# Kernel optimization log

Hardware: AMD Instinct MI355X
Metric: run time of the kernel (lower is better)

## Reference

```python
import jax, jax.numpy as jnp
import numpy as np

B, T, I, H, O = 256, 128, 2048, 128, 2


def setup_inputs() -> dict:
    key = jax.random.key(0)
    ks = jax.random.split(key, 5)
    return {
        "x": jax.random.normal(ks[0], (B, T, I), dtype=jnp.float32),
        "Wi": jax.random.normal(ks[1], (I, 4 * H), dtype=jnp.float32) / np.sqrt(I),
        "Uh": jax.random.normal(ks[2], (H, 4 * H), dtype=jnp.float32) / np.sqrt(H),
        "b": jnp.zeros((4 * H,), dtype=jnp.float32),
        "Wout": jax.random.normal(ks[3], (H, O), dtype=jnp.float32) / np.sqrt(H),
        "bout": jnp.zeros((O,), dtype=jnp.float32),
    }


def reference(x, Wi, Uh, b, Wout, bout):
    # x: [B, T, I] -> reshape(-1, T, I) is identity here
    Bx, Tx = x.shape[0], x.shape[1]
    Hh = Uh.shape[0]
    # precompute input contributions for all timesteps: [B, T, 4H]
    xg = jnp.einsum('bti,ig->btg', x, Wi)
    c0 = jnp.zeros((Bx, Hh), dtype=x.dtype)
    h0 = jnp.zeros((Bx, Hh), dtype=x.dtype)

    def step(carry, xt):
        c, h = carry
        z = xt + h @ Uh + b  # [B, 4H], flax gate order: i, f, g, o
        i, f, g, o = jnp.split(z, 4, axis=-1)
        c_new = jax.nn.sigmoid(f) * c + jax.nn.sigmoid(i) * jnp.tanh(g)
        h_new = jax.nn.sigmoid(o) * jnp.tanh(c_new)
        return (c_new, h_new), None

    (c_f, h_f), _ = jax.lax.scan(step, (c0, h0), jnp.swapaxes(xg, 0, 1))
    # final hidden state -> dense output head
    return h_f @ Wout + bout
```

## Files before the change

### kernel.cpp

```cpp
#include <hip/hip_runtime.h>

#define B_ 256
#define T_ 128
#define I_ 2048
#define H_ 128
#define G_ 512
#define O_ 2

typedef _Float16 half8 __attribute__((ext_vector_type(8)));
typedef float f32x4 __attribute__((ext_vector_type(4)));

__global__ void wt_kernel(const float* __restrict__ Wi, _Float16* __restrict__ Wt) {
    int idx = blockIdx.x * 256 + threadIdx.x;
    int n = idx >> 11;
    int k = idx & 2047;
    Wt[idx] = (_Float16)Wi[k * G_ + n];
}

#define BM 128
#define BN 128
#define BK 32
#define LDSW 40

__device__ __forceinline__ half8 pack_f16(const f32x4& a, const f32x4& b) {
    half8 r;
    r[0]=(_Float16)a[0]; r[1]=(_Float16)a[1]; r[2]=(_Float16)a[2]; r[3]=(_Float16)a[3];
    r[4]=(_Float16)b[0]; r[5]=(_Float16)b[1]; r[6]=(_Float16)b[2]; r[7]=(_Float16)b[3];
    return r;
}

__launch_bounds__(256, 2)
__global__ void gemm_xg(const float* __restrict__ X, const _Float16* __restrict__ Wt,
                        float* __restrict__ xg) {
    __shared__ _Float16 lds_a[BM * LDSW];
    __shared__ _Float16 lds_b[BN * LDSW];

    int bid = blockIdx.x;
    int swz = (bid & 7) * 128 + (bid >> 3);
    int bm = swz >> 2;
    int bn = swz & 3;
    int m0 = bm * BM, n0 = bn * BN;

    const int t = threadIdx.x;
    const int row_s = t >> 1;
    const int kh    = (t & 1) << 4;

    const float*    aptr = X  + (size_t)(m0 + row_s) * I_ + kh;
    const _Float16* bptr = Wt + (size_t)(n0 + row_s) * I_ + kh;
    const int st_off = row_s * LDSW + kh;

    const int l  = t & 63;
    const int w  = t >> 6;
    const int wm = w >> 1, wn = w & 1;
    const int lr = l & 15;
    const int kq = (l >> 4) << 3;

    f32x4 acc[4][4];
    #pragma unroll
    for (int mi = 0; mi < 4; ++mi)
        #pragma unroll
        for (int ni = 0; ni < 4; ++ni)
            acc[mi][ni] = (f32x4){0.f, 0.f, 0.f, 0.f};

    for (int kt = 0; kt < I_ / BK; ++kt) {
        const int k0 = kt * BK;
        f32x4 a0 = *(const f32x4*)(aptr + k0 + 0);
        f32x4 a1 = *(const f32x4*)(aptr + k0 + 4);
        f32x4 a2 = *(const f32x4*)(aptr + k0 + 8);
        f32x4 a3 = *(const f32x4*)(aptr + k0 + 12);
        half8 b0 = *(const half8*)(bptr + k0);
        half8 b1 = *(const half8*)(bptr + k0 + 8);
        half8 pa0 = pack_f16(a0, a1);
        half8 pa1 = pack_f16(a2, a3);

        if (kt) __syncthreads();
        *(half8*)&lds_a[st_off]     = pa0;
        *(half8*)&lds_a[st_off + 8] = pa1;
        *(half8*)&lds_b[st_off]     = b0;
        *(half8*)&lds_b[st_off + 8] = b1;
        __syncthreads();

        half8 af[4], bf[4];
        #pragma unroll
        for (int mi = 0; mi < 4; ++mi)
            af[mi] = *(const half8*)&lds_a[(wm * 64 + mi * 16 + lr) * LDSW + kq];
        #pragma unroll
        for (int ni = 0; ni < 4; ++ni)
            bf[ni] = *(const half8*)&lds_b[(wn * 64 + ni * 16 + lr) * LDSW + kq];
        #pragma unroll
        for (int mi = 0; mi < 4; ++mi)
            #pragma unroll
            for (int ni = 0; ni < 4; ++ni)
                acc[mi][ni] = __builtin_amdgcn_mfma_f32_16x16x32_f16(af[mi], bf[ni], acc[mi][ni], 0, 0, 0);
    }

    #pragma unroll
    for (int mi = 0; mi < 4; ++mi) {
        #pragma unroll
        for (int ni = 0; ni < 4; ++ni) {
            const int col = n0 + wn * 64 + ni * 16 + lr;
            #pragma unroll
            for (int r = 0; r < 4; ++r) {
                const int row = m0 + wm * 64 + mi * 16 + (l >> 4) * 4 + r;
                xg[(size_t)row * G_ + col] = acc[mi][ni][r];
            }
        }
    }
}

__device__ __forceinline__ float sigmoidf_fast(float x) {
    return 1.f / (1.f + __expf(-x));
}
__device__ __forceinline__ float tanhf_fast(float x) {
    return 1.f - 2.f / (__expf(2.f * x) + 1.f);
}

__launch_bounds__(512, 2)
__global__ void lstm_scan(const float* __restrict__ xg, const float* __restrict__ Uh,
                          const float* __restrict__ bias, const float* __restrict__ Wout,
                          const float* __restrict__ bout, float* __restrict__ out) {
    __shared__ float h_lds[H_];
    __shared__ float z_lds[G_];
    const int b = blockIdx.x;
    const int j = threadIdx.x;

    float U[H_];
    #pragma unroll
    for (int k = 0; k < H_; ++k) U[k] = Uh[k * G_ + j];
    const float bj = bias[j];
    if (j < H_) h_lds[j] = 0.f;
    float c = 0.f;
    __syncthreads();

    const float* xgb = xg + (size_t)b * T_ * G_;
    for (int t = 0; t < T_; ++t) {
        float z = xgb[t * G_ + j] + bj;
        #pragma unroll
        for (int k = 0; k < H_; k += 4) {
            f32x4 hv = *(const f32x4*)&h_lds[k];
            z += hv[0] * U[k] + hv[1] * U[k + 1] + hv[2] * U[k + 2] + hv[3] * U[k + 3];
        }
        z_lds[j] = z;
        __syncthreads();
        if (j < H_) {
            float si = sigmoidf_fast(z_lds[j]);
            float sf = sigmoidf_fast(z_lds[j + 128]);
            float tg = tanhf_fast  (z_lds[j + 256]);
            float so = sigmoidf_fast(z_lds[j + 384]);
            c = sf * c + si * tg;
            h_lds[j] = so * tanhf_fast(c);
        }
        __syncthreads();
    }

    if (j < O_) {
        float acc2 = bout[j];
        for (int k = 0; k < H_; ++k) acc2 += h_lds[k] * Wout[k * O_ + j];
        out[b * O_ + j] = acc2;
    }
}

extern "C" void kernel_launch(void* const* d_in, const int* in_sizes, int n_in,
                              void* d_out, int out_size, void* d_ws, size_t ws_size,
                              hipStream_t stream) {
    const float* x    = (const float*)d_in[0];
    const float* Wi   = (const float*)d_in[1];
    const float* Uh   = (const float*)d_in[2];
    const float* bias = (const float*)d_in[3];
    const float* Wout = (const float*)d_in[4];
    const float* bout = (const float*)d_in[5];
    float* out = (float*)d_out;

    _Float16* Wt = (_Float16*)d_ws;
    float*    xg = (float*)((char*)d_ws + (size_t)G_ * I_ * sizeof(_Float16));

    wt_kernel<<<(G_ * I_) / 256, 256, 0, stream>>>(Wi, Wt);
    gemm_xg<<<(B_ * T_ / BM) * (G_ / BN), 256, 0, stream>>>(x, Wt, xg);
    lstm_scan<<<B_, 512, 0, stream>>>(xg, Uh, bias, Wout, bout, out);
}
```

Before: 613.3 us.

## Pipeline GEMM with direct global-to-LDS loads, fp16 xg, and restructured LSTM scan

The GEMM now streams fp32 X and fp16 Wt straight into double-buffered, XOR-swizzled LDS with global_load_lds and converts X to fp16 at fragment-load time. This overlaps the next tile's loads with MFMA work and needs one barrier per K step instead of two. The xg intermediate is stored in fp16, halving its write and read traffic at the cost of some precision. The Wi transpose uses a tiled LDS kernel for coalesced access. The LSTM scan gives each thread all four gates of one hidden unit over a quarter of K and reduces with shuffles, which removes the z round trip through LDS and one barrier per step, and it prefetches the next step's xg.

```diff
diff --git a/kernel.cpp b/kernel.cpp
--- a/kernel.cpp
+++ b/kernel.cpp
@@ -1,4 +1,5 @@
 #include <hip/hip_runtime.h>
+#include <stdint.h>
 
 #define B_ 256
 #define T_ 128
@@ -10,50 +11,50 @@
 typedef _Float16 half8 __attribute__((ext_vector_type(8)));
 typedef float f32x4 __attribute__((ext_vector_type(4)));
 
-__global__ void wt_kernel(const float* __restrict__ Wi, _Float16* __restrict__ Wt) {
-    int idx = blockIdx.x * 256 + threadIdx.x;
-    int n = idx >> 11;
-    int k = idx & 2047;
-    Wt[idx] = (_Float16)Wi[k * G_ + n];
-}
-
-#define BM 128
-#define BN 128
-#define BK 32
-#define LDSW 40
-
-__device__ __forceinline__ half8 pack_f16(const f32x4& a, const f32x4& b) {
-    half8 r;
-    r[0]=(_Float16)a[0]; r[1]=(_Float16)a[1]; r[2]=(_Float16)a[2]; r[3]=(_Float16)a[3];
-    r[4]=(_Float16)b[0]; r[5]=(_Float16)b[1]; r[6]=(_Float16)b[2]; r[7]=(_Float16)b[3];
-    return r;
-}
-
-__launch_bounds__(256, 2)
+__device__ __forceinline__ void gll16(const void* g, void* l) {
+    __builtin_amdgcn_global_load_lds((const __attribute__((address_space(1))) unsigned int*)g,
+                                     (__attribute__((address_space(3))) unsigned int*)l,
+                                     16, 0, 0);
+}
+
+__global__ void wt2(const float* __restrict__ Wi, _Float16* __restrict__ Wt) {
+    __shared__ float tile[32][33];
+    const int k0 = (blockIdx.x >> 4) * 32;
+    const int n0 = (blockIdx.x & 15) * 32;
+    const int t = threadIdx.x;
+    const int r = t >> 5, c = t & 31;
+    #pragma unroll
+    for (int i = 0; i < 4; ++i)
+        tile[r + 8 * i][c] = Wi[(size_t)(k0 + r + 8 * i) * G_ + n0 + c];
+    __syncthreads();
+    #pragma unroll
+    for (int i = 0; i < 4; ++i)
+        Wt[(size_t)(n0 + r + 8 * i) * I_ + k0 + c] = (_Float16)tile[c][r + 8 * i];
+}
+
+__launch_bounds__(256, 3)
 __global__ void gemm_xg(const float* __restrict__ X, const _Float16* __restrict__ Wt,
-                        float* __restrict__ xg) {
-    __shared__ _Float16 lds_a[BM * LDSW];
-    __shared__ _Float16 lds_b[BN * LDSW];
-
-    int bid = blockIdx.x;
-    int swz = (bid & 7) * 128 + (bid >> 3);
-    int bm = swz >> 2;
-    int bn = swz & 3;
-    int m0 = bm * BM, n0 = bn * BN;
-
-    const int t = threadIdx.x;
-    const int row_s = t >> 1;
-    const int kh    = (t & 1) << 4;
-
-    const float*    aptr = X  + (size_t)(m0 + row_s) * I_ + kh;
-    const _Float16* bptr = Wt + (size_t)(n0 + row_s) * I_ + kh;
-    const int st_off = row_s * LDSW + kh;
-
-    const int l  = t & 63;
-    const int w  = t >> 6;
+                        _Float16* __restrict__ xg) {
+    __shared__ float    lds_a[2][128 * 32];
+    __shared__ _Float16 lds_b[2][128 * 32];
+
+    const int bid = blockIdx.x;
+    const int swz = (bid & 7) * 128 + (bid >> 3);
+    const int m0 = (swz >> 2) * 128;
+    const int n0 = (swz & 3) * 128;
+
+    const int tid = threadIdx.x;
+    const int l = tid & 63, w = tid >> 6;
     const int wm = w >> 1, wn = w & 1;
     const int lr = l & 15;
-    const int kq = (l >> 4) << 3;
+    const int q  = l >> 4;
+
+    const int a_unit = (l & 7) ^ (l >> 3);
+    const float* aglb = X + (size_t)(m0 + w * 32 + (l >> 3)) * I_ + a_unit * 4;
+    const int b_r4 = (l >> 2) & 3;
+    const int b_r2 = (l >> 4) & 3;
+    const int b_unit = (l & 3) ^ ((b_r4 + b_r2) & 3);
+    const _Float16* bglb = Wt + (size_t)(n0 + w * 32 + (l >> 2)) * I_ + b_unit * 8;
 
     f32x4 acc[4][4];
     #pragma unroll
@@ -62,36 +63,54 @@
         for (int ni = 0; ni < 4; ++ni)
             acc[mi][ni] = (f32x4){0.f, 0.f, 0.f, 0.f};
 
-    for (int kt = 0; kt < I_ / BK; ++kt) {
-        const int k0 = kt * BK;
-        f32x4 a0 = *(const f32x4*)(aptr + k0 + 0);
-        f32x4 a1 = *(const f32x4*)(aptr + k0 + 4);
-        f32x4 a2 = *(const f32x4*)(aptr + k0 + 8);
-        f32x4 a3 = *(const f32x4*)(aptr + k0 + 12);
-        half8 b0 = *(const half8*)(bptr + k0);
-        half8 b1 = *(const half8*)(bptr + k0 + 8);
-        half8 pa0 = pack_f16(a0, a1);
-        half8 pa1 = pack_f16(a2, a3);
-
-        if (kt) __syncthreads();
-        *(half8*)&lds_a[st_off]     = pa0;
-        *(half8*)&lds_a[st_off + 8] = pa1;
-        *(half8*)&lds_b[st_off]     = b0;
-        *(half8*)&lds_b[st_off + 8] = b1;
-        __syncthreads();
+    #pragma unroll
+    for (int cc = 0; cc < 4; ++cc)
+        gll16(aglb + (size_t)cc * 8 * I_, (char*)&lds_a[0][0] + (w * 4 + cc) * 1024);
+    #pragma unroll
+    for (int cc = 0; cc < 2; ++cc)
+        gll16(bglb + (size_t)cc * 16 * I_, (char*)&lds_b[0][0] + (w * 2 + cc) * 1024);
+    __syncthreads();
+
+    for (int kt = 0; kt < I_ / 32; ++kt) {
+        const int cur = kt & 1;
+        if (kt < I_ / 32 - 1) {
+            const int ko = (kt + 1) * 32;
+            #pragma unroll
+            for (int cc = 0; cc < 4; ++cc)
+                gll16(aglb + ko + (size_t)cc * 8 * I_,
+                      (char*)&lds_a[cur ^ 1][0] + (w * 4 + cc) * 1024);
+            #pragma unroll
+            for (int cc = 0; cc < 2; ++cc)
+                gll16(bglb + ko + (size_t)cc * 16 * I_,
+                      (char*)&lds_b[cur ^ 1][0] + (w * 2 + cc) * 1024);
+        }
 
         half8 af[4], bf[4];
         #pragma unroll
-        for (int mi = 0; mi < 4; ++mi)
-            af[mi] = *(const half8*)&lds_a[(wm * 64 + mi * 16 + lr) * LDSW + kq];
-        #pragma unroll
-        for (int ni = 0; ni < 4; ++ni)
-            bf[ni] = *(const half8*)&lds_b[(wn * 64 + ni * 16 + lr) * LDSW + kq];
+        for (int mi = 0; mi < 4; ++mi) {
+            const int row = wm * 64 + mi * 16 + lr;
+            const int plo = (2 * q) ^ (row & 7);
+            const int phi = plo ^ 1;
+            f32x4 lo = *(const f32x4*)&lds_a[cur][row * 32 + plo * 4];
+            f32x4 hi = *(const f32x4*)&lds_a[cur][row * 32 + phi * 4];
+            half8 h;
+            h[0]=(_Float16)lo[0]; h[1]=(_Float16)lo[1]; h[2]=(_Float16)lo[2]; h[3]=(_Float16)lo[3];
+            h[4]=(_Float16)hi[0]; h[5]=(_Float16)hi[1]; h[6]=(_Float16)hi[2]; h[7]=(_Float16)hi[3];
+            af[mi] = h;
+        }
+        #pragma unroll
+        for (int ni = 0; ni < 4; ++ni) {
+            const int row = wn * 64 + ni * 16 + lr;
+            const int fB = ((row & 3) + ((row >> 2) & 3)) & 3;
+            bf[ni] = *(const half8*)&lds_b[cur][row * 32 + (q ^ fB) * 8];
+        }
         #pragma unroll
         for (int mi = 0; mi < 4; ++mi)
             #pragma unroll
             for (int ni = 0; ni < 4; ++ni)
                 acc[mi][ni] = __builtin_amdgcn_mfma_f32_16x16x32_f16(af[mi], bf[ni], acc[mi][ni], 0, 0, 0);
+
+        __syncthreads();
     }
 
     #pragma unroll
@@ -101,8 +120,8 @@
             const int col = n0 + wn * 64 + ni * 16 + lr;
             #pragma unroll
             for (int r = 0; r < 4; ++r) {
-                const int row = m0 + wm * 64 + mi * 16 + (l >> 4) * 4 + r;
-                xg[(size_t)row * G_ + col] = acc[mi][ni][r];
+                const int row = m0 + wm * 64 + mi * 16 + q * 4 + r;
+                xg[(size_t)row * G_ + col] = (_Float16)acc[mi][ni][r];
             }
         }
     }
@@ -116,47 +135,81 @@
 }
 
 __launch_bounds__(512, 2)
-__global__ void lstm_scan(const float* __restrict__ xg, const float* __restrict__ Uh,
+__global__ void lstm_scan(const _Float16* __restrict__ xg, const float* __restrict__ Uh,
                           const float* __restrict__ bias, const float* __restrict__ Wout,
                           const float* __restrict__ bout, float* __restrict__ out) {
-    __shared__ float h_lds[H_];
-    __shared__ float z_lds[G_];
-    const int b = blockIdx.x;
-    const int j = threadIdx.x;
-
-    float U[H_];
-    #pragma unroll
-    for (int k = 0; k < H_; ++k) U[k] = Uh[k * G_ + j];
-    const float bj = bias[j];
-    if (j < H_) h_lds[j] = 0.f;
-    float c = 0.f;
+    __shared__ float h4[2][4][36];
+    const int t = threadIdx.x;
+    const int w = t >> 6, l = t & 63;
+    const int lr = l & 15, p = l >> 4;
+    const int j = w * 16 + lr;
+
+    float U[32][4];
+    #pragma unroll
+    for (int m = 0; m < 32; ++m)
+        #pragma unroll
+        for (int c = 0; c < 4; ++c)
+            U[m][c] = Uh[(size_t)(32 * p + m) * G_ + j + 128 * c];
+    float bj[4];
+    #pragma unroll
+    for (int c = 0; c < 4; ++c) bj[c] = bias[j + 128 * c];
+
+    for (int idx = t; idx < 2 * 4 * 36; idx += 512) ((float*)h4)[idx] = 0.f;
+
+    const _Float16* xgb = xg + (size_t)blockIdx.x * T_ * G_;
+    float xv[4], xn[4] = {0.f, 0.f, 0.f, 0.f};
+    #pragma unroll
+    for (int c = 0; c < 4; ++c) xv[c] = (float)xgb[j + 128 * c];
+    float cst = 0.f;
+    const int wslice = w >> 1;
+    const float seed = (p == 0) ? 1.f : 0.f;
     __syncthreads();
 
-    const float* xgb = xg + (size_t)b * T_ * G_;
-    for (int t = 0; t < T_; ++t) {
-        float z = xgb[t * G_ + j] + bj;
-        #pragma unroll
+    for (int tt = 0; tt < T_; ++tt) {
+        const int rb = tt & 1;
+        if (tt < T_ - 1) {
+            #pragma unroll
+            for (int c = 0; c < 4; ++c) xn[c] = (float)xgb[(size_t)(tt + 1) * G_ + j + 128 * c];
+        }
+        float z0 = seed * (xv[0] + bj[0]), z1 = seed * (xv[1] + bj[1]);
+        float z2 = seed * (xv[2] + bj[2]), z3 = seed * (xv[3] + bj[3]);
+        #pragma unroll
+        for (int i = 0; i < 8; ++i) {
+            f32x4 hv = *(const f32x4*)&h4[rb][p][i * 4];
+            #pragma unroll
+            for (int mm = 0; mm < 4; ++mm) {
+                const float hk = hv[mm];
+                z0 += hk * U[i * 4 + mm][0];
+                z1 += hk * U[i * 4 + mm][1];
+                z2 += hk * U[i * 4 + mm][2];
+                z3 += hk * U[i * 4 + mm][3];
+            }
+        }
+        z0 += __shfl_xor(z0, 16); z0 += __shfl_xor(z0, 32);
+        z1 += __shfl_xor(z1, 16); z1 += __shfl_xor(z1, 32);
+        z2 += __shfl_xor(z2, 16); z2 += __shfl_xor(z2, 32);
+        z3 += __shfl_xor(z3, 16); z3 += __shfl_xor(z3, 32);
+        const float si = sigmoidf_fast(z0);
+        const float sf = sigmoidf_fast(z1);
+        const float tg = tanhf_fast(z2);
+        const float so = sigmoidf_fast(z3);
+        cst = sf * cst + si * tg;
+        const float hn = so * tanhf_fast(cst);
+        if (p == wslice) h4[rb ^ 1][p][j & 31] = hn;
+        #pragma unroll
+        for (int c = 0; c < 4; ++c) xv[c] = xn[c];
+        __syncthreads();
+    }
+
+    if (t < O_) {
+        float a0 = 0.f, a1 = 0.f, a2 = 0.f, a3 = 0.f;
         for (int k = 0; k < H_; k += 4) {
-            f32x4 hv = *(const f32x4*)&h_lds[k];
-            z += hv[0] * U[k] + hv[1] * U[k + 1] + hv[2] * U[k + 2] + hv[3] * U[k + 3];
-        }
-        z_lds[j] = z;
-        __syncthreads();
-        if (j < H_) {
-            float si = sigmoidf_fast(z_lds[j]);
-            float sf = sigmoidf_fast(z_lds[j + 128]);
-            float tg = tanhf_fast  (z_lds[j + 256]);
-            float so = sigmoidf_fast(z_lds[j + 384]);
-            c = sf * c + si * tg;
-            h_lds[j] = so * tanhf_fast(c);
-        }
-        __syncthreads();
-    }
-
-    if (j < O_) {
-        float acc2 = bout[j];
-        for (int k = 0; k < H_; ++k) acc2 += h_lds[k] * Wout[k * O_ + j];
-        out[b * O_ + j] = acc2;
+            a0 += h4[0][(k + 0) >> 5][(k + 0) & 31] * Wout[(k + 0) * O_ + t];
+            a1 += h4[0][(k + 1) >> 5][(k + 1) & 31] * Wout[(k + 1) * O_ + t];
+            a2 += h4[0][(k + 2) >> 5][(k + 2) & 31] * Wout[(k + 2) * O_ + t];
+            a3 += h4[0][(k + 3) >> 5][(k + 3) & 31] * Wout[(k + 3) * O_ + t];
+        }
+        out[blockIdx.x * O_ + t] = a0 + a1 + a2 + a3 + bout[t];
     }
 }
 
@@ -172,9 +225,9 @@
     float* out = (float*)d_out;
 
     _Float16* Wt = (_Float16*)d_ws;
-    float*    xg = (float*)((char*)d_ws + (size_t)G_ * I_ * sizeof(_Float16));
-
-    wt_kernel<<<(G_ * I_) / 256, 256, 0, stream>>>(Wi, Wt);
-    gemm_xg<<<(B_ * T_ / BM) * (G_ / BN), 256, 0, stream>>>(x, Wt, xg);
+    _Float16* xg = (_Float16*)((char*)d_ws + (size_t)G_ * I_ * sizeof(_Float16));
+
+    wt2<<<1024, 256, 0, stream>>>(Wi, Wt);
+    gemm_xg<<<(B_ * T_ / 128) * (G_ / 128), 256, 0, stream>>>(x, Wt, xg);
     lstm_scan<<<B_, 512, 0, stream>>>(xg, Uh, bias, Wout, bout, out);
 }
```

After: 669.0 us. 9.1% more time.
